# Performance work log

Measured on AMD Instinct MI355X. Metric: run time of the kernel, lower is better.

Reference implementation:

```python
import jax, jax.numpy as jnp
import numpy as np

N_NODES = 50000
N_EDGES = 800000
D = 64
LN_EPS = 1e-5


def setup_inputs() -> dict:
    key = jax.random.key(0)
    k1, k2, k3 = jax.random.split(key, 3)
    x = jax.random.normal(k1, (N_NODES, D), dtype=jnp.float32)
    edge_index = jax.random.randint(k2, (2, N_EDGES), 0, N_NODES, dtype=jnp.int64)
    # GCNConv linear weight (no bias in lin; conv bias separate), kaiming-ish scale
    W = jax.random.normal(k3, (D, D), dtype=jnp.float32) / np.sqrt(D)
    b = jnp.zeros((D,), dtype=jnp.float32)
    # LayerNorm affine params
    gamma = jnp.ones((D,), dtype=jnp.float32)
    beta = jnp.zeros((D,), dtype=jnp.float32)
    return {"x": x, "edge_index": edge_index, "W": W, "b": b, "gamma": gamma, "beta": beta}


def reference(x, edge_index, W, b, gamma, beta):
    n = x.shape[0]
    # --- GCNConv (normalize=True, improved=False, add_self_loops=True) ---
    loops = jnp.arange(n, dtype=edge_index.dtype)
    src = jnp.concatenate([edge_index[0], loops])  # message sources j
    dst = jnp.concatenate([edge_index[1], loops])  # message targets i
    ew = jnp.ones(src.shape[0], dtype=x.dtype)
    deg = jax.ops.segment_sum(ew, dst, num_segments=n)          # in-degree incl. self-loop
    dinv = jnp.where(deg > 0, jax.lax.rsqrt(jnp.where(deg > 0, deg, 1.0)), 0.0)
    norm = dinv[src] * dinv[dst]                                 # [E+N]
    xw = x @ W                                                   # [N, D]
    z = jax.ops.segment_sum(norm[:, None] * xw[src], dst, num_segments=n) + b
    # --- identity skip connection ---
    h = x + z
    # --- norm_act_drop: LayerNorm + ReLU (dropout_prob=0) ---
    mu = jnp.mean(h, axis=-1, keepdims=True)
    var = jnp.mean((h - mu) ** 2, axis=-1, keepdims=True)
    hn = (h - mu) * jax.lax.rsqrt(var + LN_EPS)
    return jax.nn.relu(hn * gamma + beta)
```

## Files before the change

### kernel.cpp

```cpp
#include <hip/hip_runtime.h>
#include <hip/hip_fp16.h>

#define N_NODES 50000
#define N_EDGES 800000
#define D 64
#define LN_EPS 1e-5f
#define CAP 48
#define NR 8
#define RSPAN ((N_NODES + NR - 1) / NR)
#define ECHUNKS 512
#define EPC ((N_EDGES + ECHUNKS - 1) / ECHUNKS)

typedef unsigned short u16;


__global__ void prep_edges_k(const int* __restrict__ src, const int* __restrict__ dst,
                             u16* __restrict__ usrc, u16* __restrict__ udst,
                             int* __restrict__ cnt) {
    int gid = blockIdx.x * 256 + threadIdx.x;
    if (gid < N_NODES) cnt[gid] = 0;
    if (gid < N_EDGES / 4) {
        int4 s = ((const int4*)src)[gid];
        int4 d = ((const int4*)dst)[gid];
        ((uint2*)usrc)[gid] = make_uint2((unsigned)(u16)s.x | ((unsigned)(u16)s.y << 16),
                                         (unsigned)(u16)s.z | ((unsigned)(u16)s.w << 16));
        ((uint2*)udst)[gid] = make_uint2((unsigned)(u16)d.x | ((unsigned)(u16)d.y << 16),
                                         (unsigned)(u16)d.z | ((unsigned)(u16)d.w << 16));
    }
}

__global__ void fill_k(const u16* __restrict__ usrc, const u16* __restrict__ udst,
                       int* __restrict__ cnt, u16* __restrict__ ssrc) {
    int r = blockIdx.x & (NR - 1);
    int chunk = blockIdx.x >> 3;
    int lo = r * RSPAN;
    int hi = lo + RSPAN; if (hi > N_NODES) hi = N_NODES;
    int ebeg = chunk * EPC;
    int eend = ebeg + EPC; if (eend > N_EDGES) eend = N_EDGES;
    for (int e = ebeg + threadIdx.x; e < eend; e += 256) {
        int t = udst[e];
        if (t >= lo && t < hi) {
            int pos = atomicAdd(&cnt[t], 1);
            if (pos < CAP) ssrc[(size_t)t * CAP + pos] = usrc[e];
        }
    }
}

__global__ __launch_bounds__(256) void gemm_xs(const float* __restrict__ x,
                                               const float* __restrict__ W,
                                               const int* __restrict__ cnt,
                                               __half* __restrict__ xs) {
    __shared__ float xlds[D * D];
    int tid = threadIdx.x;
    int row0 = blockIdx.x * 64;

    const float4* xg = (const float4*)(x + (size_t)row0 * D);
    float4* xl4 = (float4*)xlds;
    for (int i = tid; i < D * D / 4; i += 256) {
        int grow = row0 + (i >> 4);
        xl4[i] = (grow < N_NODES) ? xg[i] : make_float4(0.f, 0.f, 0.f, 0.f);
    }

    int lane = tid & 63;
    float wcol[D];
#pragma unroll
    for (int k = 0; k < D; ++k) wcol[k] = W[k * D + lane];
    __syncthreads();

    int wv = tid >> 6;
    for (int rr = 0; rr < 16; ++rr) {
        int r = wv * 16 + rr;
        int grow = row0 + r;
        if (grow >= N_NODES) break;
        const float4* xr = (const float4*)(xlds + r * D);
        float acc = 0.f;
#pragma unroll
        for (int k4 = 0; k4 < 16; ++k4) {
            float4 xv = xr[k4];
            acc += xv.x * wcol[k4 * 4 + 0];
            acc += xv.y * wcol[k4 * 4 + 1];
            acc += xv.z * wcol[k4 * 4 + 2];
            acc += xv.w * wcol[k4 * 4 + 3];
        }
        float di = rsqrtf((float)cnt[grow] + 1.0f);
        xs[(size_t)grow * D + lane] = __float2half(di * acc);
    }
}

__global__ void agg_ln_k(const float* __restrict__ x, const __half* __restrict__ xs,
                         const int* __restrict__ cnt, const u16* __restrict__ ssrc,
                         const float* __restrict__ b, const float* __restrict__ gamma,
                         const float* __restrict__ beta, float* __restrict__ out) {
    int row = blockIdx.x * 4 + (threadIdx.x >> 6);
    if (row >= N_NODES) return;
    int lane = threadIdx.x & 63;
    int sub = lane >> 3;
    int c8  = lane & 7;

    int dc = cnt[row];
    int deg = dc < CAP ? dc : CAP;
    size_t base = (size_t)row * CAP;

    int sv[7];
    int nr = (deg > sub) ? ((deg - sub + 7) >> 3) : 0;
#pragma unroll
    for (int r2 = 0; r2 < 6; ++r2)
        if (r2 < nr) sv[r2] = ssrc[base + sub + (r2 << 3)];
    if (sub == 0) { sv[nr] = row; ++nr; }

    float4 a0 = make_float4(0.f, 0.f, 0.f, 0.f);
    float4 a1 = make_float4(0.f, 0.f, 0.f, 0.f);
#pragma unroll
    for (int r2 = 0; r2 < 7; ++r2) {
        if (r2 < nr) {
            int s = sv[r2];
            float4 raw = *(const float4*)(xs + (size_t)s * D + c8 * 8);
            const __half2* hp = (const __half2*)&raw;
            float2 p0 = __half22float2(hp[0]), p1 = __half22float2(hp[1]);
            float2 p2 = __half22float2(hp[2]), p3 = __half22float2(hp[3]);
            a0.x += p0.x; a0.y += p0.y; a0.z += p1.x; a0.w += p1.y;
            a1.x += p2.x; a1.y += p2.y; a1.z += p3.x; a1.w += p3.y;
        }
    }
#pragma unroll
    for (int o = 8; o < 64; o <<= 1) {
        a0.x += __shfl_xor(a0.x, o, 64); a0.y += __shfl_xor(a0.y, o, 64);
        a0.z += __shfl_xor(a0.z, o, 64); a0.w += __shfl_xor(a0.w, o, 64);
        a1.x += __shfl_xor(a1.x, o, 64); a1.y += __shfl_xor(a1.y, o, 64);
        a1.z += __shfl_xor(a1.z, o, 64); a1.w += __shfl_xor(a1.w, o, 64);
    }

    float di = rsqrtf((float)dc + 1.0f);

    const float4* xp = (const float4*)(x + (size_t)row * D + c8 * 8);
    float4 x0 = xp[0], x1 = xp[1];
    const float4* bp = (const float4*)(b + c8 * 8);
    float4 b0 = bp[0], b1 = bp[1];

    float h[8];
    h[0] = x0.x + di * a0.x + b0.x;
    h[1] = x0.y + di * a0.y + b0.y;
    h[2] = x0.z + di * a0.z + b0.z;
    h[3] = x0.w + di * a0.w + b0.w;
    h[4] = x1.x + di * a1.x + b1.x;
    h[5] = x1.y + di * a1.y + b1.y;
    h[6] = x1.z + di * a1.z + b1.z;
    h[7] = x1.w + di * a1.w + b1.w;

    float s_ = 0.f;
#pragma unroll
    for (int i = 0; i < 8; ++i) s_ += h[i];
#pragma unroll
    for (int o = 1; o < 64; o <<= 1) s_ += __shfl_xor(s_, o, 64);
    float mu = s_ * (1.0f / 512.0f);
    float v_ = 0.f;
    float dd[8];
#pragma unroll
    for (int i = 0; i < 8; ++i) { dd[i] = h[i] - mu; v_ += dd[i] * dd[i]; }
#pragma unroll
    for (int o = 1; o < 64; o <<= 1) v_ += __shfl_xor(v_, o, 64);
    float rstd = rsqrtf(v_ * (1.0f / 512.0f) + LN_EPS);

    if (sub == 0) {
        const float4* gp = (const float4*)(gamma + c8 * 8);
        const float4* ep = (const float4*)(beta + c8 * 8);
        float4 g0 = gp[0], g1 = gp[1];
        float4 e0 = ep[0], e1 = ep[1];
        float4 r0, r1;
        r0.x = fmaxf(dd[0] * rstd * g0.x + e0.x, 0.f);
        r0.y = fmaxf(dd[1] * rstd * g0.y + e0.y, 0.f);
        r0.z = fmaxf(dd[2] * rstd * g0.z + e0.z, 0.f);
        r0.w = fmaxf(dd[3] * rstd * g0.w + e0.w, 0.f);
        r1.x = fmaxf(dd[4] * rstd * g1.x + e1.x, 0.f);
        r1.y = fmaxf(dd[5] * rstd * g1.y + e1.y, 0.f);
        r1.z = fmaxf(dd[6] * rstd * g1.z + e1.z, 0.f);
        r1.w = fmaxf(dd[7] * rstd * g1.w + e1.w, 0.f);
        float4* op = (float4*)(out + (size_t)row * D + c8 * 8);
        op[0] = r0;
        op[1] = r1;
    }
}

extern "C" void kernel_launch(void* const* d_in, const int* in_sizes, int n_in,
                              void* d_out, int out_size, void* d_ws, size_t ws_size,
                              hipStream_t stream) {
    const float* x     = (const float*)d_in[0];
    const int*   ei    = (const int*)d_in[1];
    const float* W     = (const float*)d_in[2];
    const float* b     = (const float*)d_in[3];
    const float* gamma = (const float*)d_in[4];
    const float* beta  = (const float*)d_in[5];
    float* out = (float*)d_out;

    const int* src = ei;
    const int* dst = ei + N_EDGES;

    int*    cnt  = (int*)d_ws;
    __half* xs   = (__half*)(cnt + N_NODES);
    u16*    usrc = (u16*)(xs + (size_t)N_NODES * D);
    u16*    udst = usrc + N_EDGES;
    u16*    ssrc = udst + N_EDGES;

    prep_edges_k<<<(N_EDGES / 4 + 255) / 256, 256, 0, stream>>>(src, dst, usrc, udst, cnt);
    fill_k<<<NR * ECHUNKS, 256, 0, stream>>>(usrc, udst, cnt, ssrc);
    gemm_xs<<<(N_NODES + 63) / 64, 256, 0, stream>>>(x, W, cnt, xs);
    agg_ln_k<<<(N_NODES + 3) / 4, 256, 0, stream>>>(x, xs, cnt, ssrc, b, gamma, beta, out);
}
```

Measured before the change: 162.1 us.

## Load neighbor lists as uint4 and gather in source-tile order

Raises the per-node neighbor capacity to 64 so each 8-lane subgroup loads its 8 source ids with a single 16-byte vector load instead of scalar loads. The gather loop now makes four passes over source-index tiles of 16384 nodes, so all waves tend to touch the same region of the xs table at once. The aim is better L2 cache locality for the random feature gathers. The cost is extra predicated loop passes, a larger ssrc buffer, and a serialized outer loop.

After: 188.0 us. +16.0%, slower.

```diff
diff --git a/kernel.cpp b/kernel.cpp
--- a/kernel.cpp
+++ b/kernel.cpp
@@ -5,11 +5,13 @@
 #define N_EDGES 800000
 #define D 64
 #define LN_EPS 1e-5f
-#define CAP 48
+#define CAP 64
 #define NR 8
 #define RSPAN ((N_NODES + NR - 1) / NR)
 #define ECHUNKS 512
 #define EPC ((N_EDGES + ECHUNKS - 1) / ECHUNKS)
+#define TILE_SHIFT 14
+#define NT 4
 
 typedef unsigned short u16;
 
@@ -82,8 +84,7 @@
             acc += xv.z * wcol[k4 * 4 + 2];
             acc += xv.w * wcol[k4 * 4 + 3];
         }
-        float di = rsqrtf((float)cnt[grow] + 1.0f);
-        xs[(size_t)grow * D + lane] = __float2half(di * acc);
+        xs[(size_t)grow * D + lane] = __float2half(rsqrtf((float)cnt[grow] + 1.0f) * acc);
     }
 }
 
@@ -99,29 +100,39 @@
 
     int dc = cnt[row];
     int deg = dc < CAP ? dc : CAP;
-    size_t base = (size_t)row * CAP;
-
-    int sv[7];
-    int nr = (deg > sub) ? ((deg - sub + 7) >> 3) : 0;
-#pragma unroll
-    for (int r2 = 0; r2 < 6; ++r2)
-        if (r2 < nr) sv[r2] = ssrc[base + sub + (r2 << 3)];
-    if (sub == 0) { sv[nr] = row; ++nr; }
+    uint4 q = ((const uint4*)(ssrc + (size_t)row * CAP))[sub];
+    unsigned sv[8];
+    sv[0] = q.x & 0xffff; sv[1] = q.x >> 16;
+    sv[2] = q.y & 0xffff; sv[3] = q.y >> 16;
+    sv[4] = q.z & 0xffff; sv[5] = q.z >> 16;
+    sv[6] = q.w & 0xffff; sv[7] = q.w >> 16;
+    int nv = deg - (sub << 3);
+    nv = nv < 0 ? 0 : (nv > 8 ? 8 : nv);
 
     float4 a0 = make_float4(0.f, 0.f, 0.f, 0.f);
     float4 a1 = make_float4(0.f, 0.f, 0.f, 0.f);
-#pragma unroll
-    for (int r2 = 0; r2 < 7; ++r2) {
-        if (r2 < nr) {
-            int s = sv[r2];
-            float4 raw = *(const float4*)(xs + (size_t)s * D + c8 * 8);
-            const __half2* hp = (const __half2*)&raw;
-            float2 p0 = __half22float2(hp[0]), p1 = __half22float2(hp[1]);
-            float2 p2 = __half22float2(hp[2]), p3 = __half22float2(hp[3]);
-            a0.x += p0.x; a0.y += p0.y; a0.z += p1.x; a0.w += p1.y;
-            a1.x += p2.x; a1.y += p2.y; a1.z += p3.x; a1.w += p3.y;
+
+#define GATHER(sid)                                                             \
+    {                                                                           \
+        float4 raw = *(const float4*)(xs + (size_t)(sid) * D + c8 * 8);         \
+        const __half2* hp = (const __half2*)&raw;                               \
+        float2 p0 = __half22float2(hp[0]), p1 = __half22float2(hp[1]);          \
+        float2 p2 = __half22float2(hp[2]), p3 = __half22float2(hp[3]);          \
+        a0.x += p0.x; a0.y += p0.y; a0.z += p1.x; a0.w += p1.y;                 \
+        a1.x += p2.x; a1.y += p2.y; a1.z += p3.x; a1.w += p3.y;                 \
+    }
+
+    if (sub == 0) GATHER(row);
+
+#pragma unroll 1
+    for (int t = 0; t < NT; ++t) {
+#pragma unroll
+        for (int j = 0; j < 8; ++j) {
+            if (j < nv && (int)(sv[j] >> TILE_SHIFT) == t) GATHER(sv[j]);
         }
     }
+#undef GATHER
+
 #pragma unroll
     for (int o = 8; o < 64; o <<= 1) {
         a0.x += __shfl_xor(a0.x, o, 64); a0.y += __shfl_xor(a0.y, o, 64);
@@ -130,7 +141,7 @@
         a1.z += __shfl_xor(a1.z, o, 64); a1.w += __shfl_xor(a1.w, o, 64);
     }
 
-    float di = rsqrtf((float)dc + 1.0f);
+    float dr = rsqrtf((float)dc + 1.0f);
 
     const float4* xp = (const float4*)(x + (size_t)row * D + c8 * 8);
     float4 x0 = xp[0], x1 = xp[1];
@@ -138,14 +149,14 @@
     float4 b0 = bp[0], b1 = bp[1];
 
     float h[8];
-    h[0] = x0.x + di * a0.x + b0.x;
-    h[1] = x0.y + di * a0.y + b0.y;
-    h[2] = x0.z + di * a0.z + b0.z;
-    h[3] = x0.w + di * a0.w + b0.w;
-    h[4] = x1.x + di * a1.x + b1.x;
-    h[5] = x1.y + di * a1.y + b1.y;
-    h[6] = x1.z + di * a1.z + b1.z;
-    h[7] = x1.w + di * a1.w + b1.w;
+    h[0] = x0.x + dr * a0.x + b0.x;
+    h[1] = x0.y + dr * a0.y + b0.y;
+    h[2] = x0.z + dr * a0.z + b0.z;
+    h[3] = x0.w + dr * a0.w + b0.w;
+    h[4] = x1.x + dr * a1.x + b1.x;
+    h[5] = x1.y + dr * a1.y + b1.y;
+    h[6] = x1.z + dr * a1.z + b1.z;
+    h[7] = x1.w + dr * a1.w + b1.w;
 
     float s_ = 0.f;
 #pragma unroll
```
